# Optimization experiments

Hardware: AMD Instinct MI355X
Metric: run time of the kernel (lower is better)

## Reference

```python
import jax, jax.numpy as jnp
import numpy as np
import math

B, S, H, NH = 2, 2048, 2048, 16
HD = H // NH  # 128


def _rope_tables(seq_len, dim, base=10000.0):
    inv_freq = 1.0 / (base ** (np.arange(0, dim, 2, dtype=np.float32) / dim))
    t = np.arange(seq_len, dtype=np.float32)
    freqs = np.outer(t, inv_freq)                      # [S, dim/2]
    emb = np.concatenate([freqs, freqs], axis=-1)      # [S, dim] (HF layout)
    return jnp.asarray(np.cos(emb)), jnp.asarray(np.sin(emb))


def setup_inputs() -> dict:
    key = jax.random.key(0)
    ks = jax.random.split(key, 6)
    sc = 1.0 / math.sqrt(H)
    cos, sin = _rope_tables(S, HD)
    return {
        "hidden_states": jax.random.normal(ks[0], (B, S, H), jnp.float32),
        "wq": jax.random.normal(ks[1], (H, H), jnp.float32) * sc,
        "wk": jax.random.normal(ks[2], (H, H), jnp.float32) * sc,
        "wv": jax.random.normal(ks[3], (H, H), jnp.float32) * sc,
        "wo": jax.random.normal(ks[4], (H, H), jnp.float32) * sc,
        "cos": cos,
        "sin": sin,
        "attention_mask": jnp.ones((B, S), jnp.float32),
        "position_ids": jnp.broadcast_to(jnp.arange(S, dtype=jnp.int64), (B, S)),
    }


def _rotate_half(x):
    x1, x2 = jnp.split(x, 2, axis=-1)
    return jnp.concatenate([-x2, x1], axis=-1)


def reference(hidden_states, wq, wk, wv, wo, cos, sin, attention_mask, position_ids):
    b, s, _ = hidden_states.shape
    # projections (torch Linear: x @ W^T)
    q = (hidden_states @ wq.T).reshape(b, s, NH, HD).transpose(0, 2, 1, 3)
    k = (hidden_states @ wk.T).reshape(b, s, NH, HD).transpose(0, 2, 1, 3)
    v = (hidden_states @ wv.T).reshape(b, s, NH, HD).transpose(0, 2, 1, 3)
    # RoPE (HF apply_rotary_pos_emb): gather tables at position_ids -> [b,1,s,hd]
    c = cos[position_ids][:, None, :, :]
    sn = sin[position_ids][:, None, :, :]
    q = q * c + _rotate_half(q) * sn
    k = k * c + _rotate_half(k) * sn
    # dense attention scores [b,h,q,k]
    scores = jnp.einsum("bhqd,bhkd->bhqk", q, k) / math.sqrt(HD)
    adder = (1.0 - attention_mask)[:, None, None, :] * -10000.0
    scores = scores + adder
    probs = jax.nn.softmax(scores.astype(jnp.float32), axis=-1).astype(q.dtype)
    attn = jnp.einsum("bhqk,bhkd->bhqd", probs, v)
    attn = attn.transpose(0, 2, 1, 3).reshape(b, s, H)
    return attn @ wo.T
```

## Files before the change

kernel.cpp:

```cpp
#include <hip/hip_runtime.h>
#include <hip/hip_bf16.h>

#define B_SZ 2
#define S_LEN 2048
#define H_DIM 2048
#define N_HEAD 16
#define HD 128

using bf16 = __hip_bfloat16;
using bf16x8 = __bf16 __attribute__((ext_vector_type(8)));
using floatx4 = float __attribute__((ext_vector_type(4)));

typedef unsigned int __attribute__((address_space(1))) as1_uint;
typedef unsigned int __attribute__((address_space(3))) as3_uint;

__device__ inline void async_load16(const void* g, void* l) {
  __builtin_amdgcn_global_load_lds((const as1_uint*)g, (as3_uint*)l, 16, 0, 0);
}

__device__ inline void store_out(float* p, float v) { *p = v; }
__device__ inline void store_out(bf16* p, float v) { *p = __float2bfloat16(v); }

__global__ __launch_bounds__(256) void cast_kernel(const float* __restrict__ in,
                                                   bf16* __restrict__ out, int n4) {
  int i = blockIdx.x * 256 + threadIdx.x;
  if (i >= n4) return;
  const float4 v = ((const float4*)in)[i];
  union { bf16 h[4]; uint2 u; } o;
  o.h[0] = __float2bfloat16(v.x);
  o.h[1] = __float2bfloat16(v.y);
  o.h[2] = __float2bfloat16(v.z);
  o.h[3] = __float2bfloat16(v.w);
  ((uint2*)out)[i] = o.u;
}

__global__ __launch_bounds__(256) void cast4_kernel(
    const float* __restrict__ a, const float* __restrict__ b,
    const float* __restrict__ c_, const float* __restrict__ d_,
    bf16* __restrict__ oa, bf16* __restrict__ ob,
    bf16* __restrict__ oc, bf16* __restrict__ od) {
  int i = blockIdx.x * 256 + threadIdx.x;
  int sel = i >> 20;
  int j = i & 0xFFFFF;
  const float* src = sel == 0 ? a : sel == 1 ? b : sel == 2 ? c_ : d_;
  bf16* dst = sel == 0 ? oa : sel == 1 ? ob : sel == 2 ? oc : od;
  const float4 v = ((const float4*)src)[j];
  union { bf16 h[4]; uint2 u; } o;
  o.h[0] = __float2bfloat16(v.x);
  o.h[1] = __float2bfloat16(v.y);
  o.h[2] = __float2bfloat16(v.z);
  o.h[3] = __float2bfloat16(v.w);
  int j2 = j;
  if (sel < 2) {
    int rr = j >> 9, cq = j & 511;
    int hh = rr >> 7, dloc = rr & 127;
    int e = dloc & 63;
    int cc = (e & 15) | ((e >> 4) << 5) | (((dloc >> 6) & 1) << 4);
    j2 = (((hh << 7) + cc) << 9) + cq;
  }
  ((uint2*)dst)[j2] = o.u;
}

template <typename OutT>
__global__ __launch_bounds__(256) void gemm_bt(const bf16* __restrict__ A,
                                               const bf16* __restrict__ B,
                                               OutT* __restrict__ C,
                                               int M, int N, int K) {
  __shared__ alignas(16) bf16 As[128 * 32];
  __shared__ alignas(16) bf16 Bs[128 * 32];
  const int tid = threadIdx.x;
  const int wave = tid >> 6;
  const int lane = tid & 63;
  const int quad = lane >> 4;
  const int l16 = lane & 15;
  const int m0 = blockIdx.x * 128;
  const int n0 = blockIdx.y * 128;
  const int wm = (wave >> 1) * 64;
  const int wn = (wave & 1) * 64;

  const bf16* Ag = A + (size_t)(m0 + (tid >> 2)) * K + (tid & 3) * 8;
  const bf16* Bg = B + (size_t)(n0 + (tid >> 2)) * K + (tid & 3) * 8;
  char* AsB = (char*)As + wave * 1024;
  char* BsB = (char*)Bs + wave * 1024;
  const size_t rowskip = (size_t)64 * K;

  floatx4 acc[4][4] = {};

  for (int k0 = 0; k0 < K; k0 += 32) {
    async_load16(Ag + k0, AsB);
    async_load16(Ag + rowskip + k0, AsB + 4096);
    async_load16(Bg + k0, BsB);
    async_load16(Bg + rowskip + k0, BsB + 4096);
    __syncthreads();

    bf16x8 af[4], bfr[4];
#pragma unroll
    for (int i = 0; i < 4; i++)
      af[i] = *(const bf16x8*)&As[(wm + i * 16 + l16) * 32 + quad * 8];
#pragma unroll
    for (int j = 0; j < 4; j++)
      bfr[j] = *(const bf16x8*)&Bs[(wn + j * 16 + l16) * 32 + quad * 8];
#pragma unroll
    for (int i = 0; i < 4; i++)
#pragma unroll
      for (int j = 0; j < 4; j++)
        acc[i][j] = __builtin_amdgcn_mfma_f32_16x16x32_bf16(af[i], bfr[j], acc[i][j], 0, 0, 0);
    __syncthreads();
  }

#pragma unroll
  for (int i = 0; i < 4; i++) {
    const int row = m0 + wm + i * 16 + quad * 4;
#pragma unroll
    for (int j = 0; j < 4; j++) {
      const int col = n0 + wn + j * 16 + l16;
#pragma unroll
      for (int r = 0; r < 4; r++)
        store_out(&C[(size_t)(row + r) * N + col], acc[i][j][r]);
    }
  }
}

__global__ __launch_bounds__(256) void gemm_qk_rope(
    const bf16* __restrict__ A, const bf16* __restrict__ B, bf16* __restrict__ C,
    const float* __restrict__ cosT, const float* __restrict__ sinT,
    const int* __restrict__ pos, int K) {
  __shared__ alignas(16) bf16 As[128 * 32];
  __shared__ alignas(16) bf16 Bs[128 * 32];
  const int tid = threadIdx.x;
  const int wave = tid >> 6;
  const int lane = tid & 63;
  const int quad = lane >> 4;
  const int l16 = lane & 15;
  const int m0 = blockIdx.x * 128;
  const int n0 = blockIdx.y * 128;
  const int wm = (wave >> 1) * 64;
  const int wn = (wave & 1) * 64;

  const bf16* Ag = A + (size_t)(m0 + (tid >> 2)) * K + (tid & 3) * 8;
  const bf16* Bg = B + (size_t)(n0 + (tid >> 2)) * K + (tid & 3) * 8;
  char* AsB = (char*)As + wave * 1024;
  char* BsB = (char*)Bs + wave * 1024;
  const size_t rowskip = (size_t)64 * K;

  floatx4 acc[4][4] = {};

  for (int k0 = 0; k0 < K; k0 += 32) {
    async_load16(Ag + k0, AsB);
    async_load16(Ag + rowskip + k0, AsB + 4096);
    async_load16(Bg + k0, BsB);
    async_load16(Bg + rowskip + k0, BsB + 4096);
    __syncthreads();

    bf16x8 af[4], bfr[4];
#pragma unroll
    for (int i = 0; i < 4; i++)
      af[i] = *(const bf16x8*)&As[(wm + i * 16 + l16) * 32 + quad * 8];
#pragma unroll
    for (int j = 0; j < 4; j++)
      bfr[j] = *(const bf16x8*)&Bs[(wn + j * 16 + l16) * 32 + quad * 8];
#pragma unroll
    for (int i = 0; i < 4; i++)
#pragma unroll
      for (int j = 0; j < 4; j++)
        acc[i][j] = __builtin_amdgcn_mfma_f32_16x16x32_bf16(af[i], bfr[j], acc[i][j], 0, 0, 0);
    __syncthreads();
  }

  const float sc = (n0 < 2048) ? 0.08838834764831845f : 1.0f;
#pragma unroll
  for (int i = 0; i < 4; i++) {
    const int row0 = m0 + wm + i * 16 + quad * 4;
#pragma unroll
    for (int r = 0; r < 4; r++) {
      const int row = row0 + r;
      const int p = pos[row];
      const float* cp = cosT + (size_t)p * HD;
      const float* sp = sinT + (size_t)p * HD;
      bf16* Crow = C + (size_t)row * 4096 + n0 + wn + l16;
#pragma unroll
      for (int jp = 0; jp < 2; jp++) {
        const int d = ((wn >> 5) + jp) * 16 + l16;
        const float c = cp[d], s = sp[d];
        const float v1 = acc[i][2 * jp][r], v2 = acc[i][2 * jp + 1][r];
        Crow[jp * 32] = __float2bfloat16((v1 * c - v2 * s) * sc);
        Crow[jp * 32 + 16] = __float2bfloat16((v2 * c + v1 * s) * sc);
      }
    }
  }
}

__global__ __launch_bounds__(256, 2) void flash_attn(
    const bf16* __restrict__ QK, const bf16* __restrict__ Vt,
    const float* __restrict__ mask, bf16* __restrict__ AO) {
  __shared__ alignas(16) bf16 KP[128 * 136];
  __shared__ alignas(16) bf16 Vs[128 * 136];
  const int tid = threadIdx.x;
  const int wave = tid >> 6;
  const int lane = tid & 63;
  const int quad = lane >> 4;
  const int l16 = lane & 15;
  const int b = blockIdx.x >> 4;
  const int h = blockIdx.x & 15;
  const int q0 = blockIdx.y * 128;

  const bf16* Qb = QK + (size_t)(b * S_LEN + q0) * 4096 + h * HD;
  const bf16* Kb = QK + (size_t)(b * S_LEN) * 4096 + 2048 + h * HD;
  const bf16* Vb = Vt + (size_t)(h * HD) * 4096 + (size_t)b * S_LEN;
  const float* Mb = mask + b * S_LEN;

  bf16x8 qf[2][4];
#pragma unroll
  for (int s = 0; s < 2; s++)
#pragma unroll
    for (int kc = 0; kc < 4; kc++)
      qf[s][kc] = *(const bf16x8*)(Qb + (size_t)(wave * 32 + s * 16 + l16) * 4096 +
                                   kc * 32 + quad * 8);

  float l_i[2][4] = {};
  floatx4 O[2][8] = {};

  for (int k0 = 0; k0 < S_LEN; k0 += 128) {
    for (int i = tid; i < 2048; i += 256) {
      int r = i >> 4;
      int c = (i & 15) * 8;
      *(uint4*)&KP[r * 136 + c] = *(const uint4*)(Kb + (size_t)(k0 + r) * 4096 + c);
      *(uint4*)&Vs[r * 136 + c] = *(const uint4*)(Vb + (size_t)r * 4096 + k0 + c);
    }
    __syncthreads();

    floatx4 Sa[2][8] = {};
#pragma unroll
    for (int ct = 0; ct < 8; ct++) {
      bf16x8 kf[4];
#pragma unroll
      for (int kc = 0; kc < 4; kc++)
        kf[kc] = *(const bf16x8*)&KP[(ct * 16 + l16) * 136 + kc * 32 + quad * 8];
#pragma unroll
      for (int s = 0; s < 2; s++)
#pragma unroll
        for (int kc = 0; kc < 4; kc++)
          Sa[s][ct] = __builtin_amdgcn_mfma_f32_16x16x32_bf16(qf[s][kc], kf[kc], Sa[s][ct], 0, 0, 0);
    }
    __syncthreads();

    float addv[8];
#pragma unroll
    for (int ct = 0; ct < 8; ct++)
      addv[ct] = (1.0f - Mb[k0 + ct * 16 + l16]) * -10000.0f - 12.0f;

#pragma unroll
    for (int s = 0; s < 2; s++) {
      const int qrow = (wave * 32 + s * 16 + quad * 4) * 136;
#pragma unroll
      for (int ct = 0; ct < 8; ct++)
#pragma unroll
        for (int r = 0; r < 4; r++) {
          float p = __expf(Sa[s][ct][r] + addv[ct]);
          l_i[s][r] += p;
          KP[qrow + r * 136 + ct * 16 + l16] = __float2bfloat16(p);
        }
    }

#pragma unroll
    for (int kc = 0; kc < 4; kc++) {
      bf16x8 pa[2];
#pragma unroll
      for (int s = 0; s < 2; s++)
        pa[s] = *(const bf16x8*)&KP[(wave * 32 + s * 16 + l16) * 136 + kc * 32 + quad * 8];
#pragma unroll
      for (int dt = 0; dt < 8; dt++) {
        bf16x8 vf = *(const bf16x8*)&Vs[(dt * 16 + l16) * 136 + kc * 32 + quad * 8];
#pragma unroll
        for (int s = 0; s < 2; s++)
          O[s][dt] = __builtin_amdgcn_mfma_f32_16x16x32_bf16(pa[s], vf, O[s][dt], 0, 0, 0);
      }
    }
    __syncthreads();
  }

#pragma unroll
  for (int s = 0; s < 2; s++)
#pragma unroll
    for (int r = 0; r < 4; r++)
#pragma unroll
      for (int off = 1; off < 16; off <<= 1)
        l_i[s][r] += __shfl_xor(l_i[s][r], off);

#pragma unroll
  for (int s = 0; s < 2; s++) {
    const int qrow = q0 + wave * 32 + s * 16 + quad * 4;
#pragma unroll
    for (int r = 0; r < 4; r++) {
      float inv = 1.0f / l_i[s][r];
      bf16* outp = AO + (size_t)(b * S_LEN + qrow + r) * H_DIM + h * HD + l16;
#pragma unroll
      for (int dt = 0; dt < 8; dt++)
        outp[dt * 16] = __float2bfloat16(O[s][dt][r] * inv);
    }
  }
}

extern "C" void kernel_launch(void* const* d_in, const int* in_sizes, int n_in,
                              void* d_out, int out_size, void* d_ws, size_t ws_size,
                              hipStream_t stream) {
  const float* hs   = (const float*)d_in[0];
  const float* wq   = (const float*)d_in[1];
  const float* wk   = (const float*)d_in[2];
  const float* wv   = (const float*)d_in[3];
  const float* wo   = (const float*)d_in[4];
  const float* cosT = (const float*)d_in[5];
  const float* sinT = (const float*)d_in[6];
  const float* mask = (const float*)d_in[7];
  const int*   pos  = (const int*)d_in[8];

  char* ws = (char*)d_ws;
  bf16* Xbf  = (bf16*)ws;
  bf16* Wqkb = (bf16*)(ws + (size_t)(16 << 20));
  bf16* Wvb  = (bf16*)(ws + (size_t)(32 << 20));
  bf16* Wob  = (bf16*)(ws + (size_t)(40 << 20));
  bf16* QKm  = (bf16*)(ws + (size_t)(48 << 20));
  bf16* Vtm  = (bf16*)(ws + (size_t)(80 << 20));
  bf16* AO   = Xbf;

  cast_kernel<<<8192, 256, 0, stream>>>(hs, Xbf, 2097152);
  cast4_kernel<<<16384, 256, 0, stream>>>(wq, wk, wv, wo,
                                          Wqkb, Wqkb + (size_t)2048 * 2048, Wvb, Wob);

  gemm_qk_rope<<<dim3(32, 32), 256, 0, stream>>>(Xbf, Wqkb, QKm, cosT, sinT, pos, 2048);
  gemm_bt<bf16><<<dim3(16, 32), 256, 0, stream>>>(Wvb, Xbf, Vtm, 2048, 4096, 2048);

  flash_attn<<<dim3(32, 16), 256, 0, stream>>>(QKm, Vtm, mask, AO);

  gemm_bt<float><<<dim3(32, 16), 256, 0, stream>>>(AO, Wob, (float*)d_out, 4096, 2048, 2048);
}
```

Measured before the change: 470.7 us.

## Fuse V projection into QK-RoPE GEMM and swizzle block order for L2 reuse

Concatenates Wq, Wk, Wv into one weight buffer so a single 1536-block GEMM computes Q, K and V. The V tiles write a transposed output directly from the epilogue. Both that GEMM and the output projection now use a 1D grid remapped into groups of 8 N-blocks per M-row, so neighbouring blocks share operand tiles in L2. This removes one launch and the tail of the separate V GEMM, at the cost of a branchy epilogue and strided transposed stores.

```diff
diff --git a/kernel.cpp b/kernel.cpp
--- a/kernel.cpp
+++ b/kernel.cpp
@@ -65,7 +65,7 @@
 __global__ __launch_bounds__(256) void gemm_bt(const bf16* __restrict__ A,
                                                const bf16* __restrict__ B,
                                                OutT* __restrict__ C,
-                                               int M, int N, int K) {
+                                               int M, int N, int K, int NB) {
   __shared__ alignas(16) bf16 As[128 * 32];
   __shared__ alignas(16) bf16 Bs[128 * 32];
   const int tid = threadIdx.x;
@@ -73,8 +73,10 @@
   const int lane = tid & 63;
   const int quad = lane >> 4;
   const int l16 = lane & 15;
-  const int m0 = blockIdx.x * 128;
-  const int n0 = blockIdx.y * 128;
+  const int L = blockIdx.x;
+  const int nb = (L & 7) | (((L >> 3) % (NB >> 3)) << 3);
+  const int m0 = (L / NB) * 128;
+  const int n0 = nb * 128;
   const int wm = (wave >> 1) * 64;
   const int wn = (wave & 1) * 64;
 
@@ -121,8 +123,9 @@
   }
 }
 
-__global__ __launch_bounds__(256) void gemm_qk_rope(
-    const bf16* __restrict__ A, const bf16* __restrict__ B, bf16* __restrict__ C,
+__global__ __launch_bounds__(256) void gemm_qkv_rope(
+    const bf16* __restrict__ A, const bf16* __restrict__ B,
+    bf16* __restrict__ QKout, bf16* __restrict__ Vtout,
     const float* __restrict__ cosT, const float* __restrict__ sinT,
     const int* __restrict__ pos, int K) {
   __shared__ alignas(16) bf16 As[128 * 32];
@@ -132,8 +135,10 @@
   const int lane = tid & 63;
   const int quad = lane >> 4;
   const int l16 = lane & 15;
-  const int m0 = blockIdx.x * 128;
-  const int n0 = blockIdx.y * 128;
+  const int L = blockIdx.x;
+  const int nb = (L & 7) | (((L >> 3) % 6) << 3);
+  const int m0 = (L / 48) * 128;
+  const int n0 = nb * 128;
   const int wm = (wave >> 1) * 64;
   const int wn = (wave & 1) * 64;
 
@@ -167,24 +172,39 @@
     __syncthreads();
   }
 
-  const float sc = (n0 < 2048) ? 0.08838834764831845f : 1.0f;
-#pragma unroll
-  for (int i = 0; i < 4; i++) {
-    const int row0 = m0 + wm + i * 16 + quad * 4;
-#pragma unroll
-    for (int r = 0; r < 4; r++) {
-      const int row = row0 + r;
-      const int p = pos[row];
-      const float* cp = cosT + (size_t)p * HD;
-      const float* sp = sinT + (size_t)p * HD;
-      bf16* Crow = C + (size_t)row * 4096 + n0 + wn + l16;
-#pragma unroll
-      for (int jp = 0; jp < 2; jp++) {
-        const int d = ((wn >> 5) + jp) * 16 + l16;
-        const float c = cp[d], s = sp[d];
-        const float v1 = acc[i][2 * jp][r], v2 = acc[i][2 * jp + 1][r];
-        Crow[jp * 32] = __float2bfloat16((v1 * c - v2 * s) * sc);
-        Crow[jp * 32 + 16] = __float2bfloat16((v2 * c + v1 * s) * sc);
+  if (n0 < 4096) {
+    const float sc = (n0 < 2048) ? 0.08838834764831845f : 1.0f;
+#pragma unroll
+    for (int i = 0; i < 4; i++) {
+      const int row0 = m0 + wm + i * 16 + quad * 4;
+#pragma unroll
+      for (int r = 0; r < 4; r++) {
+        const int row = row0 + r;
+        const int p = pos[row];
+        const float* cp = cosT + (size_t)p * HD;
+        const float* sp = sinT + (size_t)p * HD;
+        bf16* Crow = QKout + (size_t)row * 4096 + n0 + wn + l16;
+#pragma unroll
+        for (int jp = 0; jp < 2; jp++) {
+          const int d = ((wn >> 5) + jp) * 16 + l16;
+          const float c = cp[d], s = sp[d];
+          const float v1 = acc[i][2 * jp][r], v2 = acc[i][2 * jp + 1][r];
+          Crow[jp * 32] = __float2bfloat16((v1 * c - v2 * s) * sc);
+          Crow[jp * 32 + 16] = __float2bfloat16((v2 * c + v1 * s) * sc);
+        }
+      }
+    }
+  } else {
+#pragma unroll
+    for (int i = 0; i < 4; i++) {
+      const int tok = m0 + wm + i * 16 + quad * 4;
+#pragma unroll
+      for (int j = 0; j < 4; j++) {
+        const int vcol = n0 - 4096 + wn + j * 16 + l16;
+        union { bf16 h[4]; uint2 u; } pk;
+#pragma unroll
+        for (int r = 0; r < 4; r++) pk.h[r] = __float2bfloat16(acc[i][j][r]);
+        *(uint2*)&Vtout[(size_t)vcol * 4096 + tok] = pk.u;
       }
     }
   }
@@ -315,22 +335,21 @@
   const int*   pos  = (const int*)d_in[8];
 
   char* ws = (char*)d_ws;
-  bf16* Xbf  = (bf16*)ws;
-  bf16* Wqkb = (bf16*)(ws + (size_t)(16 << 20));
-  bf16* Wvb  = (bf16*)(ws + (size_t)(32 << 20));
-  bf16* Wob  = (bf16*)(ws + (size_t)(40 << 20));
-  bf16* QKm  = (bf16*)(ws + (size_t)(48 << 20));
-  bf16* Vtm  = (bf16*)(ws + (size_t)(80 << 20));
-  bf16* AO   = Xbf;
+  bf16* Xbf   = (bf16*)ws;
+  bf16* Wqkvb = (bf16*)(ws + (size_t)(16 << 20));
+  bf16* Wob   = (bf16*)(ws + (size_t)(40 << 20));
+  bf16* QKm   = (bf16*)(ws + (size_t)(48 << 20));
+  bf16* Vtm   = (bf16*)(ws + (size_t)(80 << 20));
+  bf16* AO    = Xbf;
 
   cast_kernel<<<8192, 256, 0, stream>>>(hs, Xbf, 2097152);
-  cast4_kernel<<<16384, 256, 0, stream>>>(wq, wk, wv, wo,
-                                          Wqkb, Wqkb + (size_t)2048 * 2048, Wvb, Wob);
-
-  gemm_qk_rope<<<dim3(32, 32), 256, 0, stream>>>(Xbf, Wqkb, QKm, cosT, sinT, pos, 2048);
-  gemm_bt<bf16><<<dim3(16, 32), 256, 0, stream>>>(Wvb, Xbf, Vtm, 2048, 4096, 2048);
+  cast4_kernel<<<16384, 256, 0, stream>>>(
+      wq, wk, wv, wo,
+      Wqkvb, Wqkvb + (size_t)2048 * 2048, Wqkvb + (size_t)4096 * 2048, Wob);
+
+  gemm_qkv_rope<<<1536, 256, 0, stream>>>(Xbf, Wqkvb, QKm, Vtm, cosT, sinT, pos, 2048);
 
   flash_attn<<<dim3(32, 16), 256, 0, stream>>>(QKm, Vtm, mask, AO);
 
-  gemm_bt<float><<<dim3(32, 16), 256, 0, stream>>>(AO, Wob, (float*)d_out, 4096, 2048, 2048);
-}
+  gemm_bt<float><<<512, 256, 0, stream>>>(AO, Wob, (float*)d_out, 4096, 2048, 2048, 16);
+}
```

After: 466.6 us. No clear change (-0.9%).
